# Optimization experiments

Hardware: AMD Instinct MI355X
Metric: run time of the kernel (lower is better)

The kernel has to match this reference:

```python
import jax, jax.numpy as jnp
import numpy as np

B, S, H = 2, 1024, 2048
NH, NOPE, ROPE, VD = 16, 128, 64, 128
QKD = NOPE + ROPE  # 192
QLR, KVLR = 1536, 512
EPS = 1e-5


def _ln(x, w):
    # torch F.layer_norm with weight, no bias
    m = jnp.mean(x, axis=-1, keepdims=True)
    v = jnp.mean(jnp.square(x - m), axis=-1, keepdims=True)
    return (x - m) * jax.lax.rsqrt(v + EPS) * w


def _rope(x, cos, sin):
    x1, x2 = jnp.split(x, 2, axis=-1)
    return x * cos + jnp.concatenate((-x2, x1), axis=-1) * sin


def setup_inputs() -> dict:
    key = jax.random.key(0)
    ks = jax.random.split(key, 10)
    sd = 0.02
    return {
        "hidden_states": jax.random.normal(ks[0], (B, S, H), jnp.float32),
        "cos": jax.random.uniform(ks[1], (B, S, ROPE), jnp.float32),
        "sin": jax.random.uniform(ks[2], (B, S, ROPE), jnp.float32),
        "w_qa": jax.random.normal(ks[3], (QLR, H), jnp.float32) * sd,
        "q_a_ln_w": jnp.ones((QLR,), jnp.float32),
        "w_qb": jax.random.normal(ks[4], (NH * QKD, QLR), jnp.float32) * sd,
        "w_kva": jax.random.normal(ks[5], (KVLR + ROPE, H), jnp.float32) * sd,
        "kv_a_ln_w": jnp.ones((KVLR,), jnp.float32),
        "W_UK_T": jax.random.normal(ks[6], (NH, NOPE, KVLR), jnp.float32) * sd,
        "W_UV": jax.random.normal(ks[7], (NH, KVLR, VD), jnp.float32) * sd,
        "w_o": jax.random.normal(ks[8], (H, NH * VD), jnp.float32) * sd,
    }


def reference(hidden_states, cos, sin, w_qa, q_a_ln_w, w_qb, w_kva, kv_a_ln_w,
              W_UK_T, W_UV, w_o):
    b, s, _ = hidden_states.shape
    # fused mlapo: low-rank Q path + LN + RoPE
    qa = _ln(hidden_states @ w_qa.T, q_a_ln_w)            # [b,s,QLR]
    q = (qa @ w_qb.T).reshape(b, s, NH, QKD)              # [b,s,h,192]
    q_nope, q_pe = q[..., :NOPE], q[..., NOPE:]
    q_pe = _rope(q_pe, cos[:, :, None, :], sin[:, :, None, :])
    # KV low-rank path (MQA latent) + LN + RoPE on shared k_pe
    kva = hidden_states @ w_kva.T                          # [b,s,KVLR+ROPE]
    kv_c = _ln(kva[..., :KVLR], kv_a_ln_w)                 # [b,s,KVLR]
    k_pe = _rope(kva[..., KVLR:], cos, sin)                # [b,s,ROPE]
    # absorbed latent attention
    q_lat = jnp.einsum('bshd,hdl->bshl', q_nope, W_UK_T)   # [b,s,h,KVLR]
    scores = (jnp.einsum('bqhl,bkl->bhqk', q_lat, kv_c)
              + jnp.einsum('bqhr,bkr->bhqk', q_pe, k_pe)) * (1.0 / np.sqrt(QKD))
    mask = jnp.tril(jnp.ones((s, s), bool))
    scores = jnp.where(mask, scores, jnp.finfo(scores.dtype).min)
    p = jax.nn.softmax(scores, axis=-1)                    # [b,h,q,k]
    ctx = jnp.einsum('bhqk,bkl->bqhl', p, kv_c)            # [b,s,h,KVLR]
    out = jnp.einsum('bqhl,hlv->bqhv', ctx, W_UV)          # [b,s,h,VD]
    return out.reshape(b, s, NH * VD) @ w_o.T              # [b,s,H]
```

## Files before the change

### kernel.cpp

```cpp
#include <hip/hip_runtime.h>
#include <hip/hip_bf16.h>
#include <math.h>

#define BB 2
#define SS 1024
#define HH 2048
#define NHD 16
#define NOPE 128
#define ROPED 64
#define VDIM 128
#define QKD 192
#define QLR 1536
#define KVLR 512
#define EPSF 1e-5f
#define NCOMB 2176

typedef __bf16 bf16x8 __attribute__((ext_vector_type(8)));
typedef float  f32x4  __attribute__((ext_vector_type(4)));

__device__ __forceinline__ void gload_lds16(const __bf16* g, __bf16* l) {
    __builtin_amdgcn_global_load_lds(
        (const __attribute__((address_space(1))) void*)g,
        (__attribute__((address_space(3))) void*)l, 16, 0, 0);
}

__device__ __forceinline__ void swz2d(int nx, int ny, int& bx, int& by) {
    int T = nx * ny;
    int lin = blockIdx.x + nx * blockIdx.y;
    if ((T & 7) == 0) {
        int q = T >> 3;
        lin = (lin & 7) * q + (lin >> 3);
    }
    bx = lin % nx;
    by = lin / nx;
}


template<int BK>
__device__ __forceinline__ void gemm_core_dbuf(
    const __bf16* __restrict__ Ab, const __bf16* __restrict__ Bb,
    int lda, int ldb, int m0, int n0, int K, __bf16* lds, f32x4 acc[4][4])
{
    constexpr int CH    = BK / 8;
    constexpr int LPT   = CH / 2;
    constexpr int BUFE  = 256 * BK;
    constexpr int BOFF  = 128 * BK;
    constexpr int RSTEP = 2048 / BK;
    const int tid = threadIdx.x;
    const int w = tid >> 6, lane = tid & 63, quad = lane >> 4, ln = lane & 15;
    const int wm = (w >> 1) * 64, wn = (w & 1) * 64;
    const int nt = K / BK;

    const int sr  = tid / CH;
    const int spc = tid % CH;
    const int sc  = (BK == 64) ? (spc ^ (sr & 7)) : (spc ^ ((sr >> 1) & 3));
    const __bf16* gA = Ab + (size_t)(m0 + sr) * lda + sc * 8;
    const __bf16* gB = Bb + (size_t)(n0 + sr) * ldb + sc * 8;

    const int swm = (BK == 64) ? ((wm + ln) & 7) : (((wm + ln) >> 1) & 3);
    const int swn = (BK == 64) ? ((wn + ln) & 7) : (((wn + ln) >> 1) & 3);

    auto stage = [&](int buf, int kk) {
        __bf16* la = lds + buf * BUFE + w * 512;
        __bf16* lb = la + BOFF;
        const __bf16* ga = gA + kk;
        const __bf16* gb = gB + kk;
#pragma unroll
        for (int i = 0; i < LPT; ++i) {
            gload_lds16(ga + (size_t)(i * RSTEP) * lda, la + i * 2048);
            gload_lds16(gb + (size_t)(i * RSTEP) * ldb, lb + i * 2048);
        }
    };
    auto wait_stage = [&]() {
        if constexpr (BK == 64) asm volatile("s_waitcnt vmcnt(8)" ::: "memory");
        else                    asm volatile("s_waitcnt vmcnt(4)" ::: "memory");
    };

    stage(0, 0);
    stage(1, BK);
    wait_stage();
    __builtin_amdgcn_s_barrier();
    __builtin_amdgcn_sched_barrier(0);

    for (int t = 0; t < nt; ++t) {
        const int cur = t & 1;
        const __bf16* bufA = lds + cur * BUFE;
        const __bf16* bufB = bufA + BOFF;
        bf16x8 af[BK / 32][4], bv[BK / 32][4];
#pragma unroll
        for (int ks = 0; ks < BK / 32; ++ks)
#pragma unroll
            for (int i = 0; i < 4; ++i) {
                af[ks][i] = *(const bf16x8*)
                    &bufA[(wm + ln) * BK + i * 16 * BK + (((ks * 4 + quad) ^ swm) << 3)];
                bv[ks][i] = *(const bf16x8*)
                    &bufB[(wn + ln) * BK + i * 16 * BK + (((ks * 4 + quad) ^ swn) << 3)];
            }
        __builtin_amdgcn_s_setprio(1);
#pragma unroll
        for (int ks = 0; ks < BK / 32; ++ks)
#pragma unroll
            for (int mi = 0; mi < 4; ++mi)
#pragma unroll
                for (int ni = 0; ni < 4; ++ni)
                    acc[mi][ni] = __builtin_amdgcn_mfma_f32_16x16x32_bf16(
                        af[ks][mi], bv[ks][ni], acc[mi][ni], 0, 0, 0);
        __builtin_amdgcn_s_setprio(0);
        if (t + 1 < nt) {
            __builtin_amdgcn_sched_barrier(0);
            asm volatile("" ::: "memory");
            __builtin_amdgcn_s_barrier();
            asm volatile("" ::: "memory");
            if (t + 2 < nt) {
                stage(cur, (t + 2) * BK);
                wait_stage();
            } else {
                asm volatile("s_waitcnt vmcnt(0)" ::: "memory");
            }
            __builtin_amdgcn_s_barrier();
            __builtin_amdgcn_sched_barrier(0);
        }
    }
}

template<int BK>
__device__ __forceinline__ void gemm_core_tri(
    const __bf16* __restrict__ Ab, const __bf16* __restrict__ Bb,
    int lda, int ldb, int m0, int n0, int K, __bf16* lds, f32x4 acc[4][4])
{
    constexpr int CH    = BK / 8;
    constexpr int LPT   = CH / 2;
    constexpr int BUFE  = 256 * BK;
    constexpr int BOFF  = 128 * BK;
    constexpr int RSTEP = 2048 / BK;
    const int tid = threadIdx.x;
    const int w = tid >> 6, lane = tid & 63, quad = lane >> 4, ln = lane & 15;
    const int wm = (w >> 1) * 64, wn = (w & 1) * 64;
    const int nt = K / BK;

    const int sr  = tid / CH;
    const int spc = tid % CH;
    const int sc  = (BK == 64) ? (spc ^ (sr & 7)) : (spc ^ ((sr >> 1) & 3));
    const __bf16* gA = Ab + (size_t)(m0 + sr) * lda + sc * 8;
    const __bf16* gB = Bb + (size_t)(n0 + sr) * ldb + sc * 8;

    const int swm = (BK == 64) ? ((wm + ln) & 7) : (((wm + ln) >> 1) & 3);
    const int swn = (BK == 64) ? ((wn + ln) & 7) : (((wn + ln) >> 1) & 3);

    auto stage = [&](__bf16* base, int kk) {
        __bf16* la = base + w * 512;
        __bf16* lb = la + BOFF;
        const __bf16* ga = gA + kk;
        const __bf16* gb = gB + kk;
#pragma unroll
        for (int i = 0; i < LPT; ++i) {
            gload_lds16(ga + (size_t)(i * RSTEP) * lda, la + i * 2048);
            gload_lds16(gb + (size_t)(i * RSTEP) * ldb, lb + i * 2048);
        }
    };

    __bf16* p0 = lds;
    __bf16* p1 = lds + BUFE;
    __bf16* p2 = lds + 2 * BUFE;

    stage(p0, 0);
    stage(p1, BK);
    if constexpr (BK == 64) asm volatile("s_waitcnt vmcnt(8)" ::: "memory");
    else                    asm volatile("s_waitcnt vmcnt(4)" ::: "memory");
    __builtin_amdgcn_s_barrier();
    __builtin_amdgcn_sched_barrier(0);

    for (int t = 0; t < nt; ++t) {
        bf16x8 af[BK / 32][4], bv[BK / 32][4];
#pragma unroll
        for (int ks = 0; ks < BK / 32; ++ks)
#pragma unroll
            for (int i = 0; i < 4; ++i) {
                af[ks][i] = *(const bf16x8*)
                    &p0[(wm + ln) * BK + i * 16 * BK + (((ks * 4 + quad) ^ swm) << 3)];
                bv[ks][i] = *(const bf16x8*)
                    &p0[BOFF + (wn + ln) * BK + i * 16 * BK + (((ks * 4 + quad) ^ swn) << 3)];
            }
        if (t + 2 < nt) stage(p2, (t + 2) * BK);
        asm volatile("s_waitcnt lgkmcnt(0)" ::: "memory");
        __builtin_amdgcn_sched_barrier(0);
        __builtin_amdgcn_s_setprio(1);
#pragma unroll
        for (int ks = 0; ks < BK / 32; ++ks)
#pragma unroll
            for (int mi = 0; mi < 4; ++mi)
#pragma unroll
                for (int ni = 0; ni < 4; ++ni)
                    acc[mi][ni] = __builtin_amdgcn_mfma_f32_16x16x32_bf16(
                        af[ks][mi], bv[ks][ni], acc[mi][ni], 0, 0, 0);
        __builtin_amdgcn_s_setprio(0);
        if (t + 1 < nt) {
            __builtin_amdgcn_sched_barrier(0);
            if (t + 2 < nt) {
                if constexpr (BK == 64) asm volatile("s_waitcnt vmcnt(8)" ::: "memory");
                else                    asm volatile("s_waitcnt vmcnt(4)" ::: "memory");
            } else {
                asm volatile("s_waitcnt vmcnt(0)" ::: "memory");
            }
            __builtin_amdgcn_s_barrier();
            __builtin_amdgcn_sched_barrier(0);
        }
        __bf16* tmp = p0; p0 = p1; p1 = p2; p2 = tmp;
    }
}

template<bool OUT_BF16, int BK, int MINW, bool TRI>
__global__ __launch_bounds__(256, MINW) void gemm_mfma(
    const __bf16* __restrict__ A, const __bf16* __restrict__ B, void* __restrict__ Cv,
    int M, int N, int K, int lda, int ldb, int ldc,
    long long sA, long long sB, long long sC)
{
    __shared__ __bf16 lds[TRI ? 768 * BK : 512 * BK];
    const __bf16* Ab = A + (long long)blockIdx.z * sA;
    const __bf16* Bb = B + (long long)blockIdx.z * sB;
    const int tid = threadIdx.x;
    const int w = tid >> 6, lane = tid & 63, quad = lane >> 4, ln = lane & 15;
    int bx, by; swz2d(gridDim.x, gridDim.y, bx, by);
    const int m0 = by * 128, n0 = bx * 128;
    const int wm = (w >> 1) * 64, wn = (w & 1) * 64;

    f32x4 acc[4][4];
#pragma unroll
    for (int i = 0; i < 4; ++i)
#pragma unroll
        for (int j = 0; j < 4; ++j) acc[i][j] = (f32x4){0.f, 0.f, 0.f, 0.f};

    if (TRI) gemm_core_tri<BK>(Ab, Bb, lda, ldb, m0, n0, K, lds, acc);
    else     gemm_core_dbuf<BK>(Ab, Bb, lda, ldb, m0, n0, K, lds, acc);

    if (OUT_BF16) {
        __bf16* Cb = (__bf16*)Cv + (long long)blockIdx.z * sC;
#pragma unroll
        for (int mi = 0; mi < 4; ++mi)
#pragma unroll
            for (int r = 0; r < 4; ++r) {
                size_t row = (size_t)(m0 + wm + mi * 16 + quad * 4 + r);
#pragma unroll
                for (int ni = 0; ni < 4; ++ni)
                    Cb[row * ldc + (n0 + wn + ni * 16 + ln)] = (__bf16)acc[mi][ni][r];
            }
    } else {
        float* Cb = (float*)Cv + (long long)blockIdx.z * sC;
#pragma unroll
        for (int mi = 0; mi < 4; ++mi)
#pragma unroll
            for (int r = 0; r < 4; ++r) {
                size_t row = (size_t)(m0 + wm + mi * 16 + quad * 4 + r);
#pragma unroll
                for (int ni = 0; ni < 4; ++ni)
                    Cb[row * ldc + (n0 + wn + ni * 16 + ln)] = acc[mi][ni][r];
            }
    }
}

__global__ __launch_bounds__(256, 3) void gemm_qlat(
    const __bf16* __restrict__ qb, const __bf16* __restrict__ Wkb,
    __bf16* __restrict__ Qc)
{
    __shared__ __bf16 lds[768 * 32];
    const int h = blockIdx.z;
    const __bf16* Ab = qb + (size_t)h * QKD;
    const __bf16* Bb = Wkb + (size_t)h * KVLR * NOPE;
    const int tid = threadIdx.x;
    const int w = tid >> 6, lane = tid & 63, quad = lane >> 4, ln = lane & 15;
    int bx, by; swz2d(gridDim.x, gridDim.y, bx, by);
    const int m0 = by * 128, n0 = bx * 128;
    const int wm = (w >> 1) * 64, wn = (w & 1) * 64;

    f32x4 acc[4][4];
#pragma unroll
    for (int i = 0; i < 4; ++i)
#pragma unroll
        for (int j = 0; j < 4; ++j) acc[i][j] = (f32x4){0.f, 0.f, 0.f, 0.f};

    gemm_core_tri<32>(Ab, Bb, NHD * QKD, NOPE, m0, n0, NOPE, lds, acc);

#pragma unroll
    for (int mi = 0; mi < 4; ++mi)
#pragma unroll
        for (int r = 0; r < 4; ++r) {
            int row = m0 + wm + mi * 16 + quad * 4 + r;
            int bb = row >> 10, s = row & 1023;
            __bf16* dst = Qc + ((size_t)(bb * NHD + h) * SS + s) * 576;
#pragma unroll
            for (int ni = 0; ni < 4; ++ni)
                dst[n0 + wn + ni * 16 + ln] = (__bf16)acc[mi][ni][r];
        }
}

__global__ __launch_bounds__(256, 3) void gemm_scores(
    const __bf16* __restrict__ Qc, const __bf16* __restrict__ Kc,
    __bf16* __restrict__ Sc)
{
    int lin = blockIdx.x + 36 * blockIdx.y;
    lin = (lin & 7) * 144 + (lin >> 3);
    const int z = lin / 36;
    const int i = lin - z * 36;
    int mt = (int)((sqrtf(8.f * i + 1.f) - 1.f) * 0.5f);
    if (mt * (mt + 1) / 2 > i) --mt;
    if ((mt + 1) * (mt + 2) / 2 <= i) ++mt;
    const int nt = i - mt * (mt + 1) / 2;

    const int b = z >> 4;
    __shared__ __bf16 lds[768 * 32];
    const __bf16* Ab = Qc + (size_t)z * SS * 576;
    const __bf16* Bb = Kc + (size_t)b * SS * 576;
    __bf16* Cb = Sc + (size_t)z * SS * SS;
    const int tid = threadIdx.x;
    const int w = tid >> 6, lane = tid & 63, quad = lane >> 4, ln = lane & 15;
    const int m0 = mt * 128, n0 = nt * 128;
    const int wm = (w >> 1) * 64, wn = (w & 1) * 64;

    f32x4 acc[4][4];
#pragma unroll
    for (int i2 = 0; i2 < 4; ++i2)
#pragma unroll
        for (int j = 0; j < 4; ++j) acc[i2][j] = (f32x4){0.f, 0.f, 0.f, 0.f};

    gemm_core_tri<32>(Ab, Bb, 576, 576, m0, n0, 576, lds, acc);

    const float SCL2 = 0.07216878364870323f * 1.4426950408889634f;
#pragma unroll
    for (int mi = 0; mi < 4; ++mi)
#pragma unroll
        for (int r = 0; r < 4; ++r) {
            int row = m0 + wm + mi * 16 + quad * 4 + r;
#pragma unroll
            for (int ni = 0; ni < 4; ++ni) {
                int col = n0 + wn + ni * 16 + ln;
                float v = acc[mi][ni][r] * SCL2;
                if (col > row) v = -1e30f;
                Cb[(size_t)row * SS + col] = (__bf16)v;
            }
        }
}

__global__ __launch_bounds__(256) void softmax_kernel(__bf16* __restrict__ Sc)
{
    const int z = blockIdx.y;
    const int w = threadIdx.x >> 6, lane = threadIdx.x & 63;
    const int r = blockIdx.x * 4 + w;
    __bf16* row = Sc + (size_t)z * SS * SS + (size_t)r * SS;
    const int ncols = ((r >> 7) + 1) << 7;
    const int i0 = lane * 8, i1 = i0 + 512;
    const bool a0 = i0 < ncols, a1 = i1 < ncols;
    float v[16];
    float lmax = -1e30f;
    if (a0) {
        bf16x8 c = *(const bf16x8*)(row + i0);
#pragma unroll
        for (int j = 0; j < 8; ++j) { v[j] = (float)c[j]; lmax = fmaxf(lmax, v[j]); }
    }
    if (a1) {
        bf16x8 c = *(const bf16x8*)(row + i1);
#pragma unroll
        for (int j = 0; j < 8; ++j) { v[8 + j] = (float)c[j]; lmax = fmaxf(lmax, v[8 + j]); }
    }
#pragma unroll
    for (int off = 1; off < 64; off <<= 1) lmax = fmaxf(lmax, __shfl_xor(lmax, off));
    float lsum = 0.f;
    if (a0) {
#pragma unroll
        for (int j = 0; j < 8; ++j) { v[j] = __builtin_amdgcn_exp2f(v[j] - lmax); lsum += v[j]; }
    }
    if (a1) {
#pragma unroll
        for (int j = 0; j < 8; ++j) { v[8 + j] = __builtin_amdgcn_exp2f(v[8 + j] - lmax); lsum += v[8 + j]; }
    }
#pragma unroll
    for (int off = 1; off < 64; off <<= 1) lsum += __shfl_xor(lsum, off);
    const float inv = 1.f / lsum;
    if (a0) {
        bf16x8 c;
#pragma unroll
        for (int j = 0; j < 8; ++j) c[j] = (__bf16)(v[j] * inv);
        *(bf16x8*)(row + i0) = c;
    }
    if (a1) {
        bf16x8 c;
#pragma unroll
        for (int j = 0; j < 8; ++j) c[j] = (__bf16)(v[8 + j] * inv);
        *(bf16x8*)(row + i1) = c;
    }
}

__global__ __launch_bounds__(256, 3) void gemm_pv(
    const __bf16* __restrict__ Sc, const __bf16* __restrict__ Vt,
    __bf16* __restrict__ ctx)
{
    int lin = blockIdx.x + 32 * blockIdx.y;
    lin = (lin & 7) * 128 + (lin >> 3);
    const int z = lin >> 5;
    const int rem = lin & 31;
    const int mt = rem >> 2, nt = rem & 3;

    const int b = z >> 4, h = z & 15;
    const int Keff = (mt + 1) * 128;
    __shared__ __bf16 lds[768 * 32];
    const __bf16* Ab = Sc + (size_t)z * SS * SS;
    const __bf16* Bb = Vt + (size_t)b * 512 * 1024;
    const int tid = threadIdx.x;
    const int w = tid >> 6, lane = tid & 63, quad = lane >> 4, ln = lane & 15;
    const int m0 = mt * 128, n0 = nt * 128;
    const int wm = (w >> 1) * 64, wn = (w & 1) * 64;

    f32x4 acc[4][4];
#pragma unroll
    for (int i = 0; i < 4; ++i)
#pragma unroll
        for (int j = 0; j < 4; ++j) acc[i][j] = (f32x4){0.f, 0.f, 0.f, 0.f};

    gemm_core_tri<32>(Ab, Bb, SS, 1024, m0, n0, Keff, lds, acc);

#pragma unroll
    for (int mi = 0; mi < 4; ++mi)
#pragma unroll
        for (int r = 0; r < 4; ++r) {
            int row = m0 + wm + mi * 16 + quad * 4 + r;
            __bf16* op = ctx + (size_t)(b * SS + row) * (NHD * KVLR) + h * KVLR;
#pragma unroll
            for (int ni = 0; ni < 4; ++ni)
                op[n0 + wn + ni * 16 + ln] = (__bf16)acc[mi][ni][r];
        }
}

__global__ __launch_bounds__(256) void castf2b(const float* __restrict__ in,
                                               __bf16* __restrict__ out, int n)
{
    int i = (blockIdx.x * 256 + threadIdx.x) * 4;
    if (i < n) {
        float4 v = *(const float4*)(in + i);
        out[i] = (__bf16)v.x; out[i + 1] = (__bf16)v.y;
        out[i + 2] = (__bf16)v.z; out[i + 3] = (__bf16)v.w;
    }
}

__global__ __launch_bounds__(256) void cast_comb(const float* __restrict__ wqa,
                                                 const float* __restrict__ wkva,
                                                 __bf16* __restrict__ out)
{
    int idx = (blockIdx.x * 256 + threadIdx.x) * 4;
    int row = idx >> 11, col = idx & 2047;
    const float* src;
    if (row < 1536)      src = wqa + (size_t)row * 2048 + col;
    else if (row < 2112) src = wkva + (size_t)(row - 1536) * 2048 + col;
    else {
        out[idx] = (__bf16)0.f; out[idx + 1] = (__bf16)0.f;
        out[idx + 2] = (__bf16)0.f; out[idx + 3] = (__bf16)0.f;
        return;
    }
    float4 v = *(const float4*)src;
    out[idx] = (__bf16)v.x; out[idx + 1] = (__bf16)v.y;
    out[idx + 2] = (__bf16)v.z; out[idx + 3] = (__bf16)v.w;
}

__global__ __launch_bounds__(256) void transpose_cast(const float* __restrict__ in,
                                                      __bf16* __restrict__ out,
                                                      int R, int C)
{
    __shared__ float t[32][33];
    in  += (size_t)blockIdx.z * R * C;
    out += (size_t)blockIdx.z * R * C;
    int c0 = blockIdx.x * 32, r0 = blockIdx.y * 32;
    int tx = threadIdx.x & 31, ty = threadIdx.x >> 5;
#pragma unroll
    for (int i = 0; i < 4; ++i) {
        int r = ty + i * 8;
        t[r][tx] = in[(size_t)(r0 + r) * C + c0 + tx];
    }
    __syncthreads();
#pragma unroll
    for (int i = 0; i < 4; ++i) {
        int rr = ty + i * 8;
        out[(size_t)(c0 + rr) * R + r0 + tx] = (__bf16)t[tx][rr];
    }
}

__global__ __launch_bounds__(256) void transpose_kc(const __bf16* __restrict__ Kc,
                                                    __bf16* __restrict__ Vt)
{
    __shared__ __bf16 t[32][33];
    int b = blockIdx.z;
    int k0 = blockIdx.x * 32, f0 = blockIdx.y * 32;
    int tx = threadIdx.x & 31, ty = threadIdx.x >> 5;
    const __bf16* src = Kc + (size_t)b * SS * 576;
#pragma unroll
    for (int i = 0; i < 4; ++i)
        t[ty + i * 8][tx] = src[(size_t)(k0 + ty + i * 8) * 576 + f0 + tx];
    __syncthreads();
    __bf16* dst = Vt + (size_t)b * 512 * 1024;
#pragma unroll
    for (int i = 0; i < 4; ++i)
        dst[(size_t)(f0 + ty + i * 8) * 1024 + k0 + tx] = t[tx][ty + i * 8];
}

__global__ __launch_bounds__(256) void ln_kernel(const float* __restrict__ x,
                                                 const float* __restrict__ w,
                                                 __bf16* __restrict__ y, int N, int ldx)
{
    long long row = blockIdx.x;
    const float* xr = x + row * ldx;
    __bf16* yr = y + row * N;
    int tid = threadIdx.x;
    float s = 0.f, ss = 0.f;
    for (int i = tid; i < N; i += 256) { float v = xr[i]; s += v; ss += v * v; }
#pragma unroll
    for (int off = 32; off > 0; off >>= 1) { s += __shfl_down(s, off); ss += __shfl_down(ss, off); }
    __shared__ float rs[4], rss[4];
    __shared__ float smean, sinv;
    int wave = tid >> 6, lane = tid & 63;
    if (lane == 0) { rs[wave] = s; rss[wave] = ss; }
    __syncthreads();
    if (tid == 0) {
        float S = rs[0] + rs[1] + rs[2] + rs[3];
        float Q = rss[0] + rss[1] + rss[2] + rss[3];
        float mean = S / N;
        float var = Q / N - mean * mean;
        smean = mean; sinv = rsqrtf(var + EPSF);
    }
    __syncthreads();
    float mean = smean, inv = sinv;
    for (int i = tid; i < N; i += 256) yr[i] = (__bf16)((xr[i] - mean) * inv * w[i]);
}

__global__ __launch_bounds__(256) void prep_kernel(
    const float* __restrict__ kva, int ld, const float* __restrict__ kvw,
    const float* __restrict__ cosb, const float* __restrict__ sinb,
    __bf16* __restrict__ Kc, const __bf16* __restrict__ q,
    __bf16* __restrict__ Qc)
{
    long long row = blockIdx.x;
    const float* kr = kva + row * ld;
    const float* cr = cosb + row * ROPED;
    const float* sr = sinb + row * ROPED;
    int tid = threadIdx.x;
    float v0 = kr[tid], v1 = kr[tid + 256];
    float s = v0 + v1, ss = v0 * v0 + v1 * v1;
#pragma unroll
    for (int off = 32; off > 0; off >>= 1) { s += __shfl_down(s, off); ss += __shfl_down(ss, off); }
    __shared__ float rs[4], rss[4];
    __shared__ float smean, sinv;
    int wave = tid >> 6, lane = tid & 63;
    if (lane == 0) { rs[wave] = s; rss[wave] = ss; }
    __syncthreads();
    if (tid == 0) {
        float S = rs[0] + rs[1] + rs[2] + rs[3];
        float Q = rss[0] + rss[1] + rss[2] + rss[3];
        float mean = S / KVLR;
        float var = Q / KVLR - mean * mean;
        smean = mean; sinv = rsqrtf(var + EPSF);
    }
    __syncthreads();
    float mean = smean, inv = sinv;
    __bf16* kc = Kc + row * 576;
    kc[tid]       = (__bf16)((v0 - mean) * inv * kvw[tid]);
    kc[tid + 256] = (__bf16)((v1 - mean) * inv * kvw[tid + 256]);
    if (tid < 32) {
        float x1 = kr[KVLR + tid], x2 = kr[KVLR + 32 + tid];
        kc[512 + tid]      = (__bf16)(x1 * cr[tid] - x2 * sr[tid]);
        kc[512 + 32 + tid] = (__bf16)(x2 * cr[32 + tid] + x1 * sr[32 + tid]);
    }
    const int bb = (int)(row >> 10), sp = (int)(row & 1023);
    const __bf16* qr = q + row * (NHD * QKD);
#pragma unroll
    for (int j = 0; j < 2; ++j) {
        int idx = tid + j * 256;
        int h = idx >> 5, p = idx & 31;
        const __bf16* base = qr + h * QKD + NOPE;
        float x1 = (float)base[p], x2 = (float)base[32 + p];
        __bf16* qcb = Qc + ((size_t)(bb * NHD + h) * SS + sp) * 576 + 512;
        qcb[p]      = (__bf16)(x1 * cr[p] - x2 * sr[p]);
        qcb[32 + p] = (__bf16)(x2 * cr[32 + p] + x1 * sr[32 + p]);
    }
}

extern "C" void kernel_launch(void* const* d_in, const int* in_sizes, int n_in,
                              void* d_out, int out_size, void* d_ws, size_t ws_size,
                              hipStream_t stream)
{
    const float* hidden    = (const float*)d_in[0];
    const float* cosb      = (const float*)d_in[1];
    const float* sinb      = (const float*)d_in[2];
    const float* w_qa      = (const float*)d_in[3];
    const float* q_a_ln_w  = (const float*)d_in[4];
    const float* w_qb      = (const float*)d_in[5];
    const float* w_kva     = (const float*)d_in[6];
    const float* kv_a_ln_w = (const float*)d_in[7];
    const float* W_UK_T    = (const float*)d_in[8];
    const float* W_UV      = (const float*)d_in[9];
    const float* w_o       = (const float*)d_in[10];
    float* out = (float*)d_out;

    const int M = BB * SS;
    float*  qakva = (float*)d_ws;
    __bf16* Xb    = (__bf16*)(qakva + (size_t)M * NCOMB);
    __bf16* qab   = Xb    + (size_t)M * HH;
    __bf16* qb    = qab   + (size_t)M * QLR;
    __bf16* qlatb = qb    + (size_t)M * NHD * QKD;
    __bf16* Sc    = (__bf16*)d_ws;
    __bf16* Kc    = qlatb + (size_t)M * NHD * KVLR;
    __bf16* Qc    = Kc    + (size_t)M * 576;
    __bf16* Vt    = Qc    + (size_t)M * NHD * 576;
    __bf16* ctxb  = Vt    + (size_t)BB * 512 * SS;
    __bf16* ohb   = ctxb  + (size_t)M * NHD * KVLR;
    __bf16* w_cmb = ohb   + (size_t)M * HH;
    __bf16* w_qbb = w_cmb + (size_t)NCOMB * HH;
    __bf16* Wkb   = w_qbb + (size_t)NHD * QKD * QLR;
    __bf16* Wvb   = Wkb   + (size_t)NHD * KVLR * NOPE;
    __bf16* w_ob  = Wvb   + (size_t)NHD * VDIM * KVLR;

    dim3 blk(256);

    castf2b<<<dim3((M * HH) / 1024), blk, 0, stream>>>(hidden, Xb, M * HH);
    cast_comb<<<dim3((NCOMB * HH) / 1024), blk, 0, stream>>>(w_qa, w_kva, w_cmb);
    castf2b<<<dim3((NHD * QKD * QLR) / 1024), blk, 0, stream>>>(w_qb, w_qbb, NHD * QKD * QLR);
    castf2b<<<dim3((HH * HH) / 1024), blk, 0, stream>>>(w_o, w_ob, HH * HH);
    transpose_cast<<<dim3(KVLR / 32, NOPE / 32, NHD), blk, 0, stream>>>(W_UK_T, Wkb, NOPE, KVLR);
    transpose_cast<<<dim3(VDIM / 32, KVLR / 32, NHD), blk, 0, stream>>>(W_UV, Wvb, KVLR, VDIM);

    gemm_mfma<false, 64, 2, false><<<dim3(NCOMB / 128, M / 128, 1), blk, 0, stream>>>(
        Xb, w_cmb, qakva, M, NCOMB, HH, HH, HH, NCOMB, 0, 0, 0);
    ln_kernel<<<dim3(M), blk, 0, stream>>>(qakva, q_a_ln_w, qab, QLR, NCOMB);
    gemm_mfma<true, 64, 2, false><<<dim3(NHD * QKD / 128, M / 128, 1), blk, 0, stream>>>(
        qab, w_qbb, qb, M, NHD * QKD, QLR, QLR, QLR, NHD * QKD, 0, 0, 0);
    prep_kernel<<<dim3(M), blk, 0, stream>>>(qakva + QLR, NCOMB, kv_a_ln_w,
                                             cosb, sinb, Kc, qb, Qc);
    transpose_kc<<<dim3(SS / 32, 512 / 32, BB), blk, 0, stream>>>(Kc, Vt);
    gemm_qlat<<<dim3(KVLR / 128, M / 128, NHD), blk, 0, stream>>>(qb, Wkb, Qc);
    gemm_scores<<<dim3(36, 32), blk, 0, stream>>>(Qc, Kc, Sc);
    softmax_kernel<<<dim3(SS / 4, 32), blk, 0, stream>>>(Sc);
    gemm_pv<<<dim3(32, 32), blk, 0, stream>>>(Sc, Vt, ctxb);
    gemm_mfma<true, 32, 3, true><<<dim3(VDIM / 128, M / 128, NHD), blk, 0, stream>>>(
        ctxb, Wvb, ohb, M, VDIM, KVLR,
        NHD * KVLR, KVLR, NHD * VDIM,
        (long long)KVLR, (long long)VDIM * KVLR, (long long)VDIM);
    gemm_mfma<false, 64, 2, false><<<dim3(HH / 128, M / 128, 1), blk, 0, stream>>>(
        ohb, w_ob, out, M, HH, NHD * VDIM, NHD * VDIM, NHD * VDIM, HH, 0, 0, 0);
}
```

Measured before the change: 331.9 us.

## Reassociate W_UV before PV to shrink the attention-value GEMM

```diff
diff --git a/kernel.cpp b/kernel.cpp
--- a/kernel.cpp
+++ b/kernel.cpp
@@ -34,7 +34,6 @@
     bx = lin % nx;
     by = lin / nx;
 }
-
 
 template<int BK>
 __device__ __forceinline__ void gemm_core_dbuf(
@@ -293,6 +292,44 @@
         }
 }
 
+__global__ __launch_bounds__(256, 3) void gemm_vh(
+    const __bf16* __restrict__ Wvb, const __bf16* __restrict__ Kc,
+    __bf16* __restrict__ Vh)
+{
+    int lin = blockIdx.x + 8 * blockIdx.z;
+    lin = (lin & 7) * 32 + (lin >> 3);
+    const int z = lin >> 3;
+    const int ntile = lin & 7;
+    const int b = z >> 4, h = z & 15;
+
+    __shared__ __bf16 lds[768 * 32];
+    const __bf16* Ab = Wvb + (size_t)h * VDIM * KVLR;
+    const __bf16* Bb = Kc + (size_t)b * SS * 576;
+    const int tid = threadIdx.x;
+    const int w = tid >> 6, lane = tid & 63, quad = lane >> 4, ln = lane & 15;
+    const int m0 = 0, n0 = ntile * 128;
+    const int wm = (w >> 1) * 64, wn = (w & 1) * 64;
+
+    f32x4 acc[4][4];
+#pragma unroll
+    for (int i = 0; i < 4; ++i)
+#pragma unroll
+        for (int j = 0; j < 4; ++j) acc[i][j] = (f32x4){0.f, 0.f, 0.f, 0.f};
+
+    gemm_core_tri<32>(Ab, Bb, KVLR, 576, m0, n0, KVLR, lds, acc);
+
+    __bf16* Cb = Vh + (size_t)z * VDIM * SS;
+#pragma unroll
+    for (int mi = 0; mi < 4; ++mi)
+#pragma unroll
+        for (int r = 0; r < 4; ++r) {
+            int row = m0 + wm + mi * 16 + quad * 4 + r;
+#pragma unroll
+            for (int ni = 0; ni < 4; ++ni)
+                Cb[(size_t)row * SS + (n0 + wn + ni * 16 + ln)] = (__bf16)acc[mi][ni][r];
+        }
+}
+
 __global__ __launch_bounds__(256, 3) void gemm_scores(
     const __bf16* __restrict__ Qc, const __bf16* __restrict__ Kc,
     __bf16* __restrict__ Sc)
@@ -390,23 +427,22 @@
 }
 
 __global__ __launch_bounds__(256, 3) void gemm_pv(
-    const __bf16* __restrict__ Sc, const __bf16* __restrict__ Vt,
-    __bf16* __restrict__ ctx)
-{
-    int lin = blockIdx.x + 32 * blockIdx.y;
-    lin = (lin & 7) * 128 + (lin >> 3);
-    const int z = lin >> 5;
-    const int rem = lin & 31;
-    const int mt = rem >> 2, nt = rem & 3;
+    const __bf16* __restrict__ Sc, const __bf16* __restrict__ Vh,
+    __bf16* __restrict__ ohb)
+{
+    int lin = blockIdx.x + 8 * blockIdx.y;
+    lin = (lin & 7) * 32 + (lin >> 3);
+    const int z = lin >> 3;
+    const int mt = lin & 7;
 
     const int b = z >> 4, h = z & 15;
     const int Keff = (mt + 1) * 128;
     __shared__ __bf16 lds[768 * 32];
     const __bf16* Ab = Sc + (size_t)z * SS * SS;
-    const __bf16* Bb = Vt + (size_t)b * 512 * 1024;
+    const __bf16* Bb = Vh + (size_t)z * VDIM * SS;
     const int tid = threadIdx.x;
     const int w = tid >> 6, lane = tid & 63, quad = lane >> 4, ln = lane & 15;
-    const int m0 = mt * 128, n0 = nt * 128;
+    const int m0 = mt * 128, n0 = 0;
     const int wm = (w >> 1) * 64, wn = (w & 1) * 64;
 
     f32x4 acc[4][4];
@@ -415,14 +451,14 @@
 #pragma unroll
         for (int j = 0; j < 4; ++j) acc[i][j] = (f32x4){0.f, 0.f, 0.f, 0.f};
 
-    gemm_core_tri<32>(Ab, Bb, SS, 1024, m0, n0, Keff, lds, acc);
+    gemm_core_tri<32>(Ab, Bb, SS, SS, m0, n0, Keff, lds, acc);
 
 #pragma unroll
     for (int mi = 0; mi < 4; ++mi)
 #pragma unroll
         for (int r = 0; r < 4; ++r) {
             int row = m0 + wm + mi * 16 + quad * 4 + r;
-            __bf16* op = ctx + (size_t)(b * SS + row) * (NHD * KVLR) + h * KVLR;
+            __bf16* op = ohb + (size_t)(b * SS + row) * (NHD * VDIM) + h * VDIM;
 #pragma unroll
             for (int ni = 0; ni < 4; ++ni)
                 op[n0 + wn + ni * 16 + ln] = (__bf16)acc[mi][ni][r];
@@ -479,24 +515,6 @@
         int rr = ty + i * 8;
         out[(size_t)(c0 + rr) * R + r0 + tx] = (__bf16)t[tx][rr];
     }
-}
-
-__global__ __launch_bounds__(256) void transpose_kc(const __bf16* __restrict__ Kc,
-                                                    __bf16* __restrict__ Vt)
-{
-    __shared__ __bf16 t[32][33];
-    int b = blockIdx.z;
-    int k0 = blockIdx.x * 32, f0 = blockIdx.y * 32;
-    int tx = threadIdx.x & 31, ty = threadIdx.x >> 5;
-    const __bf16* src = Kc + (size_t)b * SS * 576;
-#pragma unroll
-    for (int i = 0; i < 4; ++i)
-        t[ty + i * 8][tx] = src[(size_t)(k0 + ty + i * 8) * 576 + f0 + tx];
-    __syncthreads();
-    __bf16* dst = Vt + (size_t)b * 512 * 1024;
-#pragma unroll
-    for (int i = 0; i < 4; ++i)
-        dst[(size_t)(f0 + ty + i * 8) * 1024 + k0 + tx] = t[tx][ty + i * 8];
 }
 
 __global__ __launch_bounds__(256) void ln_kernel(const float* __restrict__ x,
@@ -607,6 +625,7 @@
     __bf16* Qc    = Kc    + (size_t)M * 576;
     __bf16* Vt    = Qc    + (size_t)M * NHD * 576;
     __bf16* ctxb  = Vt    + (size_t)BB * 512 * SS;
+    __bf16* Vh    = ctxb;
     __bf16* ohb   = ctxb  + (size_t)M * NHD * KVLR;
     __bf16* w_cmb = ohb   + (size_t)M * HH;
     __bf16* w_qbb = w_cmb + (size_t)NCOMB * HH;
@@ -630,15 +649,11 @@
         qab, w_qbb, qb, M, NHD * QKD, QLR, QLR, QLR, NHD * QKD, 0, 0, 0);
     prep_kernel<<<dim3(M), blk, 0, stream>>>(qakva + QLR, NCOMB, kv_a_ln_w,
                                              cosb, sinb, Kc, qb, Qc);
-    transpose_kc<<<dim3(SS / 32, 512 / 32, BB), blk, 0, stream>>>(Kc, Vt);
+    gemm_vh<<<dim3(8, 1, 32), blk, 0, stream>>>(Wvb, Kc, Vh);
     gemm_qlat<<<dim3(KVLR / 128, M / 128, NHD), blk, 0, stream>>>(qb, Wkb, Qc);
     gemm_scores<<<dim3(36, 32), blk, 0, stream>>>(Qc, Kc, Sc);
     softmax_kernel<<<dim3(SS / 4, 32), blk, 0, stream>>>(Sc);
-    gemm_pv<<<dim3(32, 32), blk, 0, stream>>>(Sc, Vt, ctxb);
-    gemm_mfma<true, 32, 3, true><<<dim3(VDIM / 128, M / 128, NHD), blk, 0, stream>>>(
-        ctxb, Wvb, ohb, M, VDIM, KVLR,
-        NHD * KVLR, KVLR, NHD * VDIM,
-        (long long)KVLR, (long long)VDIM * KVLR, (long long)VDIM);
+    gemm_pv<<<dim3(8, 32), blk, 0, stream>>>(Sc, Vh, ohb);
     gemm_mfma<false, 64, 2, false><<<dim3(HH / 128, M / 128, 1), blk, 0, stream>>>(
         ohb, w_ob, out, M, HH, NHD * VDIM, NHD * VDIM, NHD * VDIM, HH, 0, 0, 0);
 }
```

New measurement: 311.3 us. 6.2% less time.
